# Performance work log

Hardware: AMD Instinct MI355X
Metric: run time of the kernel (lower is better)

## Reference

```python
import jax, jax.numpy as jnp
import numpy as np

N_NODES = 50000
N_EDGES = 600000
D = 128
NUM_GRAPHS = 64


def gcn_conv(x, W, b, edge_index, edge_weight, n):
    """PyG GCNConv: y = D^-1/2 (A+I) D^-1/2 (x W) + b, with self-loop weight 1."""
    h = x @ W  # [n, out]
    src, dst = edge_index[0], edge_index[1]
    if edge_weight is None:
        edge_weight = jnp.ones(src.shape, dtype=x.dtype)
    # append self loops
    loop = jnp.arange(n)
    src_f = jnp.concatenate([src, loop])
    dst_f = jnp.concatenate([dst, loop])
    w_f = jnp.concatenate([edge_weight, jnp.ones((n,), dtype=x.dtype)])
    deg = jax.ops.segment_sum(w_f, dst_f, num_segments=n)
    dis = jnp.where(deg > 0, jax.lax.rsqrt(jnp.maximum(deg, 1e-12)), 0.0)
    norm = dis[src_f] * w_f * dis[dst_f]  # [E+n]
    msg = h[src_f] * norm[:, None]
    out = jax.ops.segment_sum(msg, dst_f, num_segments=n)
    return out + b


def setup_inputs() -> dict:
    key = jax.random.key(0)
    ks = jax.random.split(key, 24)
    def w(k, shape, scale=0.05):
        return jax.random.normal(k, shape, dtype=jnp.float32) * scale
    inp = {
        'x': jax.random.normal(ks[0], (N_NODES, D), dtype=jnp.float32),
        'edge_index': jax.random.randint(ks[1], (2, N_EDGES), 0, N_NODES),
        'edge_attr': jax.random.uniform(ks[2], (N_EDGES, 4), dtype=jnp.float32),
        'batch': jnp.sort(jax.random.randint(ks[3], (N_NODES,), 0, NUM_GRAPHS)),
        'W1A': w(ks[4], (D, D)), 'b1A': jnp.zeros((D,), jnp.float32),
        'W1B': w(ks[5], (D, D)), 'b1B': jnp.zeros((D,), jnp.float32),
        'W1C': w(ks[6], (D, D)), 'b1C': jnp.zeros((D,), jnp.float32),
        'W1D': w(ks[7], (D, D)), 'b1D': jnp.zeros((D,), jnp.float32),
        'W2': w(ks[8], (4 * D, 2 * D)), 'b2': jnp.zeros((2 * D,), jnp.float32),
        'W3': w(ks[9], (2 * D, D)), 'b3': jnp.zeros((D,), jnp.float32),
        'Wm1': w(ks[10], (2 * D, 8)), 'bm1': jnp.zeros((8,), jnp.float32),
        'Wm2': w(ks[11], (8, 2)), 'bm2': jnp.zeros((2,), jnp.float32),
    }
    return inp


def reference(x, edge_index, edge_attr, batch, W1A, b1A, W1B, b1B, W1C, b1C,
              W1D, b1D, W2, b2, W3, b3, Wm1, bm1, Wm2, bm2):
    n = x.shape[0]
    xA = jax.nn.relu(gcn_conv(x, W1A, b1A, edge_index, edge_attr[:, 0], n))
    xB = jax.nn.relu(gcn_conv(x, W1B, b1B, edge_index, edge_attr[:, 1], n))
    xC = jax.nn.relu(gcn_conv(x, W1C, b1C, edge_index, edge_attr[:, 2], n))
    xD = jax.nn.relu(gcn_conv(x, W1D, b1D, edge_index, edge_attr[:, 3], n))
    h = jnp.concatenate([xA, xB, xC, xD], axis=1)  # [n, 4D]
    h = jax.nn.relu(gcn_conv(h, W2, b2, edge_index, None, n))
    h = gcn_conv(h, W3, b3, edge_index, None, n)  # [n, D]
    # global mean / max pool over graphs
    counts = jax.ops.segment_sum(jnp.ones((n,), h.dtype), batch, num_segments=NUM_GRAPHS)
    sums = jax.ops.segment_sum(h, batch, num_segments=NUM_GRAPHS)
    mean = sums / jnp.maximum(counts, 1.0)[:, None]
    mx = jax.ops.segment_max(h, batch, num_segments=NUM_GRAPHS)
    mx = jnp.where(counts[:, None] > 0, mx, 0.0)
    g = jnp.concatenate([mean, mx], axis=1)  # [G, 2D]
    # dropout is identity in eval mode
    logits = jax.nn.relu(g @ Wm1 + bm1) @ Wm2 + bm2
    return logits
```

## Files before the change

### kernel.cpp

```cpp
#include <hip/hip_runtime.h>

#define DEV_INLINE __device__ __forceinline__

typedef __attribute__((ext_vector_type(8))) short bf16x8;
typedef __attribute__((ext_vector_type(4))) float floatx4;

DEV_INLINE unsigned fencode(float f) {
  unsigned u = __float_as_uint(f);
  return (u & 0x80000000u) ? ~u : (u | 0x80000000u);
}
DEV_INLINE float fdecode(unsigned k) {
  return __uint_as_float((k & 0x80000000u) ? (k ^ 0x80000000u) : ~k);
}

DEV_INLINE unsigned short bf16_rne(float x) {
  unsigned u = __float_as_uint(x);
  unsigned r = (u + 0x7FFFu + ((u >> 16) & 1u)) >> 16;
  return (unsigned short)r;
}
DEV_INLINE float bf2f(unsigned short u) {
  return __uint_as_float(((unsigned)u) << 16);
}

#pragma clang diagnostic ignored "-Waddress-space-conversion"
DEV_INLINE void gload_lds16(const void* g, void* l) {
  __builtin_amdgcn_global_load_lds(
      (const __attribute__((address_space(1))) unsigned int*)g,
      (__attribute__((address_space(3))) unsigned int*)l, 16, 0, 0);
}

__global__ __launch_bounds__(256)
void prep_kernel(const float* __restrict__ WA, const float* __restrict__ WB,
                 const float* __restrict__ WC, const float* __restrict__ WD,
                 const float* __restrict__ bA, const float* __restrict__ bB,
                 const float* __restrict__ bC, const float* __restrict__ bD,
                 const float* __restrict__ W2, const float* __restrict__ W3,
                 unsigned short* __restrict__ W1t, unsigned short* __restrict__ W2t,
                 unsigned short* __restrict__ W3t, float* __restrict__ biascat,
                 const float* __restrict__ x, unsigned short* __restrict__ xb,
                 int total4) {
  int i = blockIdx.x * 256 + threadIdx.x;
  if (i < 65536) {
    int z = i >> 14, rem = i & 16383, j = rem >> 7, k = rem & 127;
    const float* W = (z == 0) ? WA : (z == 1) ? WB : (z == 2) ? WC : WD;
    W1t[i] = bf16_rne(W[k * 128 + j]);
  } else if (i < 196608) {
    int i2 = i - 65536, j = i2 >> 9, k = i2 & 511;
    W2t[i2] = bf16_rne(W2[k * 256 + j]);
  } else if (i < 229376) {
    int i3 = i - 196608, j = i3 >> 8, k = i3 & 255;
    W3t[i3] = bf16_rne(W3[k * 128 + j]);
  } else if (i < 229888) {
    int i4 = i - 229376, c = i4 >> 7, j = i4 & 127;
    const float* b = (c == 0) ? bA : (c == 1) ? bB : (c == 2) ? bC : bD;
    biascat[i4] = b[j];
  }
  if (i < total4) {
    float4 v = ((const float4*)x)[i];
    ushort4 o;
    o.x = bf16_rne(v.x); o.y = bf16_rne(v.y); o.z = bf16_rne(v.z); o.w = bf16_rne(v.w);
    ((ushort4*)xb)[i] = o;
  }
}

__global__ __launch_bounds__(256)
void hist_kernel(const int* __restrict__ ei, int* __restrict__ cnt, int E) {
  int e = blockIdx.x * 256 + threadIdx.x;
  if (e < E) atomicAdd(&cnt[ei[E + e]], 1);
}

__global__ __launch_bounds__(256)
void scan1_kernel(const int* __restrict__ cnt, int* __restrict__ local,
                  int* __restrict__ bsum, int n) {
  __shared__ int s[256];
  int tid = threadIdx.x;
  int i = blockIdx.x * 256 + tid;
  int v = (i < n) ? cnt[i] : 0;
  s[tid] = v;
  __syncthreads();
#pragma unroll
  for (int off = 1; off < 256; off <<= 1) {
    int t = (tid >= off) ? s[tid - off] : 0;
    __syncthreads();
    s[tid] += t;
    __syncthreads();
  }
  if (i < n) local[i] = s[tid] - v;
  if (tid == 255) bsum[blockIdx.x] = s[255];
}

__global__ __launch_bounds__(256)
void scan2_kernel(int* __restrict__ bsum, int nb) {
  __shared__ int s[256];
  int tid = threadIdx.x;
  int v = (tid < nb) ? bsum[tid] : 0;
  s[tid] = v;
  __syncthreads();
#pragma unroll
  for (int off = 1; off < 256; off <<= 1) {
    int t = (tid >= off) ? s[tid - off] : 0;
    __syncthreads();
    s[tid] += t;
    __syncthreads();
  }
  if (tid < nb) bsum[tid] = s[tid] - v;
}

__global__ __launch_bounds__(256)
void scan3_kernel(const int* __restrict__ local, const int* __restrict__ bsum,
                  int* __restrict__ rowptr, int* __restrict__ rowwork, int n, int E) {
  int i = blockIdx.x * 256 + threadIdx.x;
  if (i < n) {
    int rp = local[i] + bsum[blockIdx.x];
    rowptr[i] = rp;
    rowwork[i] = rp;
  }
  if (i == 0) rowptr[n] = E;
}

__global__ __launch_bounds__(256)
void fill_kernel(const int* __restrict__ ei, const float* __restrict__ eattr,
                 int* __restrict__ rowwork, int* __restrict__ csr_src,
                 int* __restrict__ csr_dst, float4* __restrict__ csr_w, int E) {
  int e = blockIdx.x * 256 + threadIdx.x;
  if (e >= E) return;
  int d = ei[E + e];
  int pos = atomicAdd(&rowwork[d], 1);
  csr_src[pos] = ei[e];
  csr_dst[pos] = d;
  csr_w[pos] = ((const float4*)eattr)[e];
}

__global__ __launch_bounds__(256)
void degcsr_kernel(const int* __restrict__ rowptr, const float4* __restrict__ csr_w,
                   float* __restrict__ dis, int n) {
  int d = blockIdx.x * 256 + threadIdx.x;
  if (d >= n) return;
  int beg = rowptr[d], end = rowptr[d + 1];
  float s0 = 1.f, s1 = 1.f, s2 = 1.f, s3 = 1.f;
  for (int i = beg; i < end; ++i) {
    float4 w = csr_w[i];
    s0 += w.x; s1 += w.y; s2 += w.z; s3 += w.w;
  }
  dis[d]         = 1.0f / sqrtf(s0);
  dis[n + d]     = 1.0f / sqrtf(s1);
  dis[2 * n + d] = 1.0f / sqrtf(s2);
  dis[3 * n + d] = 1.0f / sqrtf(s3);
  dis[4 * n + d] = 1.0f / sqrtf(1.0f + (float)(end - beg));
}

__global__ __launch_bounds__(256)
void edgeprep_kernel(const int* __restrict__ csr_src, const int* __restrict__ csr_dst,
                     const float4* __restrict__ csr_w, const float* __restrict__ dis,
                     float4* __restrict__ norm4, float* __restrict__ norm1,
                     int n, int E) {
  int i = blockIdx.x * 256 + threadIdx.x;
  if (i >= E) return;
  int s = csr_src[i], d = csr_dst[i];
  float4 w = csr_w[i];
  float4 o;
  o.x = dis[s] * w.x * dis[d];
  o.y = dis[n + s] * w.y * dis[n + d];
  o.z = dis[2 * n + s] * w.z * dis[2 * n + d];
  o.w = dis[3 * n + s] * w.w * dis[3 * n + d];
  norm4[i] = o;
  norm1[i] = dis[4 * n + s] * dis[4 * n + d];
}

__global__ __launch_bounds__(256)
void agg4x_kernel(const unsigned short* __restrict__ xb,
                  unsigned short* __restrict__ xa,
                  const int* __restrict__ rowptr, const int* __restrict__ csr_src,
                  const float4* __restrict__ norm4, const float* __restrict__ dis,
                  int n, int npad) {
  int d = blockIdx.x * 4 + (threadIdx.x >> 6);
  if (d >= n) return;
  int t = threadIdx.x & 63;
  float dc0 = dis[d], dc1 = dis[n + d], dc2 = dis[2 * n + d], dc3 = dis[3 * n + d];
  const ushort2* x2 = (const ushort2*)xb;
  ushort2 xu = x2[(size_t)d * 64 + t];
  float xvx = bf2f(xu.x), xvy = bf2f(xu.y);
  float a0x = xvx * dc0 * dc0, a0y = xvy * dc0 * dc0;
  float a1x = xvx * dc1 * dc1, a1y = xvy * dc1 * dc1;
  float a2x = xvx * dc2 * dc2, a2y = xvy * dc2 * dc2;
  float a3x = xvx * dc3 * dc3, a3y = xvy * dc3 * dc3;
  int beg = rowptr[d], end = rowptr[d + 1];
  int i = beg;
  for (; i + 4 <= end; i += 4) {
    int s0 = csr_src[i], s1 = csr_src[i + 1], s2 = csr_src[i + 2], s3 = csr_src[i + 3];
    float4 m0 = norm4[i], m1 = norm4[i + 1], m2 = norm4[i + 2], m3 = norm4[i + 3];
    ushort2 u0 = x2[(size_t)s0 * 64 + t];
    ushort2 u1 = x2[(size_t)s1 * 64 + t];
    ushort2 u2 = x2[(size_t)s2 * 64 + t];
    ushort2 u3 = x2[(size_t)s3 * 64 + t];
    float h0x = bf2f(u0.x), h0y = bf2f(u0.y);
    float h1x = bf2f(u1.x), h1y = bf2f(u1.y);
    float h2x = bf2f(u2.x), h2y = bf2f(u2.y);
    float h3x = bf2f(u3.x), h3y = bf2f(u3.y);
    a0x += h0x * m0.x; a0y += h0y * m0.x;
    a1x += h0x * m0.y; a1y += h0y * m0.y;
    a2x += h0x * m0.z; a2y += h0y * m0.z;
    a3x += h0x * m0.w; a3y += h0y * m0.w;
    a0x += h1x * m1.x; a0y += h1y * m1.x;
    a1x += h1x * m1.y; a1y += h1y * m1.y;
    a2x += h1x * m1.z; a2y += h1y * m1.z;
    a3x += h1x * m1.w; a3y += h1y * m1.w;
    a0x += h2x * m2.x; a0y += h2y * m2.x;
    a1x += h2x * m2.y; a1y += h2y * m2.y;
    a2x += h2x * m2.z; a2y += h2y * m2.z;
    a3x += h2x * m2.w; a3y += h2y * m2.w;
    a0x += h3x * m3.x; a0y += h3y * m3.x;
    a1x += h3x * m3.y; a1y += h3y * m3.y;
    a2x += h3x * m3.z; a2y += h3y * m3.z;
    a3x += h3x * m3.w; a3y += h3y * m3.w;
  }
  for (; i < end; ++i) {
    int s = csr_src[i];
    float4 m = norm4[i];
    ushort2 u = x2[(size_t)s * 64 + t];
    float hx = bf2f(u.x), hy = bf2f(u.y);
    a0x += hx * m.x; a0y += hy * m.x;
    a1x += hx * m.y; a1y += hy * m.y;
    a2x += hx * m.z; a2y += hy * m.z;
    a3x += hx * m.w; a3y += hy * m.w;
  }
  size_t plane = (size_t)npad * 128;
  size_t base = (size_t)d * 128 + 2 * t;
  float vx[4] = {a0x, a1x, a2x, a3x};
  float vy[4] = {a0y, a1y, a2y, a3y};
#pragma unroll
  for (int z = 0; z < 4; ++z) {
    ushort2 ov; ov.x = bf16_rne(vx[z]); ov.y = bf16_rne(vy[z]);
    *(ushort2*)&xa[plane * z + base] = ov;
  }
}

template <int MODE>
DEV_INLINE void gemm_mfma_body(const unsigned short* __restrict__ A, int K,
                               const unsigned short* __restrict__ B,
                               int ldc, int col0, unsigned short* __restrict__ Cb,
                               const float* __restrict__ bias, int M, int row0) {
  __shared__ __align__(16) unsigned short As[2][128 * 32];
  __shared__ __align__(16) unsigned short Bs[2][128 * 32];
  int tid = threadIdx.x;
  int w = tid >> 6, lane = tid & 63;
  int quad = lane >> 4, lrow = lane & 15;
  int wm = (w >> 1) * 64, wn = (w & 1) * 64;

  floatx4 acc[4][4];
#pragma unroll
  for (int i = 0; i < 4; ++i)
#pragma unroll
    for (int j = 0; j < 4; ++j) acc[i][j] = {0.f, 0.f, 0.f, 0.f};

  auto stage = [&](int b, int k0) {
#pragma unroll
    for (int half = 0; half < 2; ++half) {
      int row = half * 64 + lane;
      int lb = (w * 128 + half * 64) * 8;
      gload_lds16(A + (size_t)(row0 + row) * K + k0 + w * 8, &As[b][lb]);
      gload_lds16(B + (size_t)row * K + k0 + w * 8, &Bs[b][lb]);
    }
  };

  int nk = K >> 5;
  stage(0, 0);
  int buf = 0;
  for (int kt = 0; kt < nk; ++kt) {
    __syncthreads();
    if (kt + 1 < nk) stage(buf ^ 1, (kt + 1) * 32);
    bf16x8 a_[4], b_[4];
#pragma unroll
    for (int i = 0; i < 4; ++i)
      a_[i] = *(const bf16x8*)&As[buf][(quad * 128 + wm + i * 16 + lrow) * 8];
#pragma unroll
    for (int j = 0; j < 4; ++j)
      b_[j] = *(const bf16x8*)&Bs[buf][(quad * 128 + wn + j * 16 + lrow) * 8];
#pragma unroll
    for (int j = 0; j < 4; ++j)
#pragma unroll
      for (int i = 0; i < 4; ++i)
        acc[i][j] = __builtin_amdgcn_mfma_f32_16x16x32_bf16(a_[i], b_[j], acc[i][j], 0, 0, 0);
    buf ^= 1;
  }
#pragma unroll
  for (int i = 0; i < 4; ++i) {
#pragma unroll
    for (int j = 0; j < 4; ++j) {
      int colL = wn + j * 16 + lrow;
#pragma unroll
      for (int r = 0; r < 4; ++r) {
        int row = row0 + wm + i * 16 + quad * 4 + r;
        if (row < M) {
          float v = acc[i][j][r];
          if (MODE == 1) v = fmaxf(v + bias[colL], 0.0f);
          Cb[(size_t)row * ldc + col0 + colL] = bf16_rne(v);
        }
      }
    }
  }
}

__global__ __launch_bounds__(256)
void gemm_l1_mfma(const unsigned short* __restrict__ xa,
                  const unsigned short* __restrict__ W1t,
                  const float* __restrict__ biascat,
                  unsigned short* __restrict__ h1, int M, int npad) {
  int z = blockIdx.z;
  gemm_mfma_body<1>(xa + (size_t)z * npad * 128, 128, W1t + z * 16384,
                    512, z * 128, h1, biascat + z * 128, M, blockIdx.x * 128);
}

__global__ __launch_bounds__(256)
void gemm_bf16out(const unsigned short* __restrict__ A, int K,
                  const unsigned short* __restrict__ B,
                  unsigned short* __restrict__ Cb, int ldc, int M) {
  gemm_mfma_body<2>(A, K, B + (size_t)blockIdx.y * 128 * K, ldc,
                    blockIdx.y * 128, Cb, nullptr, M, blockIdx.x * 128);
}

__global__ __launch_bounds__(512)
void gemm_l2_wide(const unsigned short* __restrict__ A,
                  const unsigned short* __restrict__ B,
                  unsigned short* __restrict__ Cb, int M) {
  constexpr int K = 512;
  __shared__ __align__(16) unsigned short As[2][128 * 32];
  __shared__ __align__(16) unsigned short Bs[2][256 * 32];
  int tid = threadIdx.x;
  int w = tid >> 6, lane = tid & 63;
  int quad = lane >> 4, lrow = lane & 15;
  int wm = (w >> 2) * 64, wn = (w & 3) * 64;
  int row0 = blockIdx.x * 128;
  int u0 = w * 64;

  floatx4 acc[4][4];
#pragma unroll
  for (int i = 0; i < 4; ++i)
#pragma unroll
    for (int j = 0; j < 4; ++j) acc[i][j] = {0.f, 0.f, 0.f, 0.f};

  auto stage = [&](int b, int k0) {
    gload_lds16(A + (size_t)(row0 + (tid & 127)) * K + k0 + (tid >> 7) * 8,
                &As[b][u0 * 8]);
#pragma unroll
    for (int inst = 0; inst < 2; ++inst) {
      int u = inst * 512 + tid;
      gload_lds16(B + (size_t)(u & 255) * K + k0 + (u >> 8) * 8,
                  &Bs[b][(inst * 512 + u0) * 8]);
    }
  };

  stage(0, 0);
  int buf = 0;
#pragma unroll 1
  for (int kt = 0; kt < 16; ++kt) {
    __syncthreads();
    if (kt + 1 < 16) stage(buf ^ 1, (kt + 1) * 32);
    bf16x8 a_[4], b_[4];
#pragma unroll
    for (int i = 0; i < 4; ++i)
      a_[i] = *(const bf16x8*)&As[buf][(quad * 128 + wm + i * 16 + lrow) * 8];
#pragma unroll
    for (int j = 0; j < 4; ++j)
      b_[j] = *(const bf16x8*)&Bs[buf][(quad * 256 + wn + j * 16 + lrow) * 8];
#pragma unroll
    for (int j = 0; j < 4; ++j)
#pragma unroll
      for (int i = 0; i < 4; ++i)
        acc[i][j] = __builtin_amdgcn_mfma_f32_16x16x32_bf16(a_[i], b_[j], acc[i][j], 0, 0, 0);
    buf ^= 1;
  }
#pragma unroll
  for (int i = 0; i < 4; ++i) {
#pragma unroll
    for (int j = 0; j < 4; ++j) {
      int colL = wn + j * 16 + lrow;
#pragma unroll
      for (int r = 0; r < 4; ++r) {
        int row = row0 + wm + i * 16 + quad * 4 + r;
        if (row < M) Cb[(size_t)row * 256 + colL] = bf16_rne(acc[i][j][r]);
      }
    }
  }
}

template <int VEC, bool RELU, int OMODE>
__global__ __launch_bounds__(256)
void agg1_kernel(const unsigned short* __restrict__ hb, float* __restrict__ out,
                 unsigned short* __restrict__ ob,
                 const int* __restrict__ rowptr, const int* __restrict__ csr_src,
                 const float* __restrict__ norm1, const float* __restrict__ dis1,
                 const float* __restrict__ bias, int n) {
  constexpr int DOUT = VEC * 64;
  int d = blockIdx.x * 4 + (threadIdx.x >> 6);
  if (d >= n) return;
  int t = threadIdx.x & 63;
  float dd = dis1[d];
  float acc[VEC];
  {
    float sw = dd * dd;
#pragma unroll
    for (int k = 0; k < VEC; ++k) acc[k] = bf2f(hb[(size_t)d * DOUT + t * VEC + k]) * sw;
  }
  int beg = rowptr[d], end = rowptr[d + 1];
  int i = beg;
  for (; i + 4 <= end; i += 4) {
    int s0 = csr_src[i], s1 = csr_src[i + 1], s2 = csr_src[i + 2], s3 = csr_src[i + 3];
    float m0 = norm1[i], m1 = norm1[i + 1], m2 = norm1[i + 2], m3 = norm1[i + 3];
    if (VEC == 4) {
      ushort4 u0 = *(const ushort4*)&hb[(size_t)s0 * DOUT + t * 4];
      ushort4 u1 = *(const ushort4*)&hb[(size_t)s1 * DOUT + t * 4];
      ushort4 u2 = *(const ushort4*)&hb[(size_t)s2 * DOUT + t * 4];
      ushort4 u3 = *(const ushort4*)&hb[(size_t)s3 * DOUT + t * 4];
      acc[0] += bf2f(u0.x) * m0; acc[1] += bf2f(u0.y) * m0;
      acc[2 % VEC] += bf2f(u0.z) * m0; acc[3 % VEC] += bf2f(u0.w) * m0;
      acc[0] += bf2f(u1.x) * m1; acc[1] += bf2f(u1.y) * m1;
      acc[2 % VEC] += bf2f(u1.z) * m1; acc[3 % VEC] += bf2f(u1.w) * m1;
      acc[0] += bf2f(u2.x) * m2; acc[1] += bf2f(u2.y) * m2;
      acc[2 % VEC] += bf2f(u2.z) * m2; acc[3 % VEC] += bf2f(u2.w) * m2;
      acc[0] += bf2f(u3.x) * m3; acc[1] += bf2f(u3.y) * m3;
      acc[2 % VEC] += bf2f(u3.z) * m3; acc[3 % VEC] += bf2f(u3.w) * m3;
    } else {
      ushort2 u0 = *(const ushort2*)&hb[(size_t)s0 * DOUT + t * 2];
      ushort2 u1 = *(const ushort2*)&hb[(size_t)s1 * DOUT + t * 2];
      ushort2 u2 = *(const ushort2*)&hb[(size_t)s2 * DOUT + t * 2];
      ushort2 u3 = *(const ushort2*)&hb[(size_t)s3 * DOUT + t * 2];
      acc[0] += bf2f(u0.x) * m0; acc[1 % VEC] += bf2f(u0.y) * m0;
      acc[0] += bf2f(u1.x) * m1; acc[1 % VEC] += bf2f(u1.y) * m1;
      acc[0] += bf2f(u2.x) * m2; acc[1 % VEC] += bf2f(u2.y) * m2;
      acc[0] += bf2f(u3.x) * m3; acc[1 % VEC] += bf2f(u3.y) * m3;
    }
  }
  for (; i < end; ++i) {
    int s = csr_src[i];
    float nrm = norm1[i];
    if (VEC == 4) {
      ushort4 u = *(const ushort4*)&hb[(size_t)s * DOUT + t * 4];
      acc[0] += bf2f(u.x) * nrm; acc[1] += bf2f(u.y) * nrm;
      acc[2 % VEC] += bf2f(u.z) * nrm; acc[3 % VEC] += bf2f(u.w) * nrm;
    } else {
      ushort2 u = *(const ushort2*)&hb[(size_t)s * DOUT + t * 2];
      acc[0] += bf2f(u.x) * nrm; acc[1 % VEC] += bf2f(u.y) * nrm;
    }
  }
#pragma unroll
  for (int k = 0; k < VEC; ++k) {
    float r = acc[k] + bias[t * VEC + k];
    if (RELU) r = fmaxf(r, 0.0f);
    if (OMODE == 1) {
      ob[(size_t)d * DOUT + t * VEC + k] = bf16_rne(r);
    } else {
      out[(size_t)d * DOUT + t * VEC + k] = r;
    }
  }
}

__global__ __launch_bounds__(128)
void pool_kernel(const float* __restrict__ h3, const int* __restrict__ batch,
                 float* __restrict__ gsum, unsigned* __restrict__ gmax, int n) {
  int c = threadIdx.x;
  int start = blockIdx.x * 32;
  int end = min(start + 32, n);
  int curg = -1;
  float s = 0.0f, m = -3.402823466e38f;
  for (int i = start; i < end; ++i) {
    int g = batch[i];
    if (g != curg) {
      if (curg >= 0) {
        atomicAdd(&gsum[curg * 128 + c], s);
        atomicMax(&gmax[curg * 128 + c], fencode(m));
      }
      curg = g; s = 0.0f; m = -3.402823466e38f;
    }
    float v = h3[(size_t)i * 128 + c];
    s += v;
    m = fmaxf(m, v);
  }
  if (curg >= 0) {
    atomicAdd(&gsum[curg * 128 + c], s);
    atomicMax(&gmax[curg * 128 + c], fencode(m));
  }
}

__global__ __launch_bounds__(512)
void mlp_kernel(const float* __restrict__ gsum, const unsigned* __restrict__ gmax,
                const int* __restrict__ batch, int n, const float* __restrict__ Wm1,
                const float* __restrict__ bm1, const float* __restrict__ Wm2,
                const float* __restrict__ bm2, float* __restrict__ out) {
  __shared__ float hid[64][8];
  int t = threadIdx.x;
  int gi = t >> 3, u = t & 7;
  auto lb = [&](int key) {
    int lo = 0, hi = n;
    while (lo < hi) {
      int mid = (lo + hi) >> 1;
      if (batch[mid] < key) lo = mid + 1; else hi = mid;
    }
    return lo;
  };
  int cnt = lb(gi + 1) - lb(gi);
  float inv = 1.0f / fmaxf((float)cnt, 1.0f);
  float s = bm1[u];
  for (int k = 0; k < 128; ++k) {
    float mean = gsum[gi * 128 + k] * inv;
    s += mean * Wm1[k * 8 + u];
  }
  for (int k = 0; k < 128; ++k) {
    float mx = (cnt > 0) ? fdecode(gmax[gi * 128 + k]) : 0.0f;
    s += mx * Wm1[(128 + k) * 8 + u];
  }
  hid[gi][u] = fmaxf(s, 0.0f);
  __syncthreads();
  if (t < 128) {
    int g2 = t >> 1, o = t & 1;
    float s2 = bm2[o];
#pragma unroll
    for (int uu = 0; uu < 8; ++uu) s2 += hid[g2][uu] * Wm2[uu * 2 + o];
    out[g2 * 2 + o] = s2;
  }
}

extern "C" void kernel_launch(void* const* d_in, const int* in_sizes, int n_in,
                              void* d_out, int out_size, void* d_ws, size_t ws_size,
                              hipStream_t stream) {
  const float* x     = (const float*)d_in[0];
  const int*   ei    = (const int*)d_in[1];
  const float* eattr = (const float*)d_in[2];
  const int*   batch = (const int*)d_in[3];
  const float* W1A = (const float*)d_in[4],  *b1A = (const float*)d_in[5];
  const float* W1B = (const float*)d_in[6],  *b1B = (const float*)d_in[7];
  const float* W1C = (const float*)d_in[8],  *b1C = (const float*)d_in[9];
  const float* W1D = (const float*)d_in[10], *b1D = (const float*)d_in[11];
  const float* W2  = (const float*)d_in[12], *b2  = (const float*)d_in[13];
  const float* W3  = (const float*)d_in[14], *b3  = (const float*)d_in[15];
  const float* Wm1 = (const float*)d_in[16], *bm1 = (const float*)d_in[17];
  const float* Wm2 = (const float*)d_in[18], *bm2 = (const float*)d_in[19];
  float* out = (float*)d_out;

  const int n = in_sizes[0] / 128;
  const int E = in_sizes[1] / 2;
  const int npad = (n + 127) & ~127;
  const int nmb = npad / 128;

  char* ws = (char*)d_ws;
  size_t off = 0;
  auto alloc = [&](size_t bytes) -> void* {
    void* p = ws + off;
    off += (bytes + 255) & ~(size_t)255;
    return p;
  };

  float*    dis     = (float*)alloc((size_t)5 * n * 4);
  int*      rowptr  = (int*)alloc(((size_t)n + 1) * 4);
  int*      rowwork = (int*)alloc((size_t)n * 4);
  int*      local   = (int*)alloc((size_t)n * 4);
  int*      bsum    = (int*)alloc(256 * 4);
  size_t zoff = off;
  int*      cnt     = (int*)alloc((size_t)n * 4);
  float*    gsum    = (float*)alloc(64 * 128 * 4);
  unsigned* gmax    = (unsigned*)alloc(64 * 128 * 4);
  size_t zbytes = off - zoff;
  int*      csr_src = (int*)alloc((size_t)E * 4);
  int*      csr_dst = (int*)alloc((size_t)E * 4);
  float4*   csr_w   = (float4*)alloc((size_t)E * 16);
  float4*   norm4   = (float4*)alloc((size_t)E * 16);
  float*    norm1   = (float*)alloc((size_t)E * 4);
  unsigned short* W1t = (unsigned short*)alloc(65536 * 2);
  unsigned short* W2t = (unsigned short*)alloc(131072 * 2);
  unsigned short* W3t = (unsigned short*)alloc(32768 * 2);
  float*    biascat = (float*)alloc(512 * 4);
  unsigned short* xb   = (unsigned short*)alloc((size_t)npad * 128 * 2);
  unsigned short* bufA = (unsigned short*)alloc((size_t)npad * 512 * 2);
  unsigned short* bufB = (unsigned short*)alloc((size_t)npad * 512 * 2);
  alloc(4096);

  unsigned short* xa      = bufA;
  unsigned short* h1      = bufB;
  unsigned short* h2pre_b = bufA;
  unsigned short* h2      = bufB;
  unsigned short* h3pre_b = bufA;
  float*          h3      = (float*)(bufB + (size_t)npad * 256);

  hipMemsetAsync(ws + zoff, 0, zbytes, stream);

  int total4 = n * 32;
  prep_kernel<<<(total4 + 255) / 256, 256, 0, stream>>>(
      W1A, W1B, W1C, W1D, b1A, b1B, b1C, b1D, W2, W3,
      W1t, W2t, W3t, biascat, x, xb, total4);

  int nb = (n + 255) / 256;
  hist_kernel<<<(E + 255) / 256, 256, 0, stream>>>(ei, cnt, E);
  scan1_kernel<<<nb, 256, 0, stream>>>(cnt, local, bsum, n);
  scan2_kernel<<<1, 256, 0, stream>>>(bsum, nb);
  scan3_kernel<<<nb, 256, 0, stream>>>(local, bsum, rowptr, rowwork, n, E);
  fill_kernel<<<(E + 255) / 256, 256, 0, stream>>>(ei, eattr, rowwork, csr_src, csr_dst, csr_w, E);
  degcsr_kernel<<<(n + 255) / 256, 256, 0, stream>>>(rowptr, csr_w, dis, n);
  edgeprep_kernel<<<(E + 255) / 256, 256, 0, stream>>>(csr_src, csr_dst, csr_w,
                                                       dis, norm4, norm1, n, E);

  int nodeblk = (n + 3) / 4;
  agg4x_kernel<<<nodeblk, 256, 0, stream>>>(xb, xa, rowptr, csr_src, norm4, dis, n, npad);
  gemm_l1_mfma<<<dim3(nmb, 1, 4), 256, 0, stream>>>(xa, W1t, biascat, h1, n, npad);
  gemm_l2_wide<<<nmb, 512, 0, stream>>>(h1, W2t, h2pre_b, n);
  agg1_kernel<4, true, 1><<<nodeblk, 256, 0, stream>>>(h2pre_b, nullptr, h2,
                                                       rowptr, csr_src, norm1,
                                                       dis + (size_t)4 * n, b2, n);
  gemm_bf16out<<<dim3(nmb, 1), 256, 0, stream>>>(h2, 256, W3t, h3pre_b, 128, n);
  agg1_kernel<2, false, 0><<<nodeblk, 256, 0, stream>>>(h3pre_b, h3, nullptr,
                                                        rowptr, csr_src, norm1,
                                                        dis + (size_t)4 * n, b3, n);

  pool_kernel<<<(n + 31) / 32, 128, 0, stream>>>(h3, batch, gsum, gmax, n);
  mlp_kernel<<<1, 512, 0, stream>>>(gsum, gmax, batch, n, Wm1, bm1, Wm2, bm2, out);
}
```

Before: 477.3 us.

## Specialize layer-1 GEMM with full-K LDS load and split layer-2 aggregation

Layer-1 GEMM gets its own kernel that loads the whole K=128 A and B tiles into LDS at once, with no double-buffered k-loop, and applies bias+ReLU inline. The layer-2 aggregation over 256 columns is split into two 128-column passes with a stride parameter, which shrinks the per-row gather footprint and may improve cache locality. The final aggregation now writes bf16 instead of fp32, and pooling reads bf16, which halves that traffic at some cost in precision. The bigger LDS footprint (64KB per block) can lower occupancy for the GEMM, and the second pass re-reads the CSR arrays.

```diff
diff --git a/kernel.cpp b/kernel.cpp
--- a/kernel.cpp
+++ b/kernel.cpp
@@ -235,11 +235,79 @@
   }
 }
 
-template <int MODE>
-DEV_INLINE void gemm_mfma_body(const unsigned short* __restrict__ A, int K,
-                               const unsigned short* __restrict__ B,
-                               int ldc, int col0, unsigned short* __restrict__ Cb,
-                               const float* __restrict__ bias, int M, int row0) {
+__global__ __launch_bounds__(256)
+void gemm_l1_mfma(const unsigned short* __restrict__ xa,
+                  const unsigned short* __restrict__ W1t,
+                  const float* __restrict__ biascat,
+                  unsigned short* __restrict__ h1, int M, int npad) {
+  int z = blockIdx.z;
+  const unsigned short* A = xa + (size_t)z * npad * 128;
+  const unsigned short* B = W1t + z * 16384;
+  __shared__ __align__(16) unsigned short As[128 * 128];
+  __shared__ __align__(16) unsigned short Bs[128 * 128];
+  int tid = threadIdx.x;
+  int w = tid >> 6, lane = tid & 63;
+  int quad = lane >> 4, lrow = lane & 15;
+  int wm = (w >> 1) * 64, wn = (w & 1) * 64;
+  int row0 = blockIdx.x * 128;
+
+#pragma unroll
+  for (int u4q = 0; u4q < 4; ++u4q) {
+    int u4 = w * 4 + u4q;
+#pragma unroll
+    for (int half = 0; half < 2; ++half) {
+      int row = half * 64 + lane;
+      int lb = (u4 * 128 + half * 64) * 8;
+      gload_lds16(A + (size_t)(row0 + row) * 128 + u4 * 8, &As[lb]);
+      gload_lds16(B + (size_t)row * 128 + u4 * 8, &Bs[lb]);
+    }
+  }
+  __syncthreads();
+
+  floatx4 acc[4][4];
+#pragma unroll
+  for (int i = 0; i < 4; ++i)
+#pragma unroll
+    for (int j = 0; j < 4; ++j) acc[i][j] = {0.f, 0.f, 0.f, 0.f};
+
+#pragma unroll
+  for (int kc = 0; kc < 4; ++kc) {
+    bf16x8 a_[4], b_[4];
+#pragma unroll
+    for (int i = 0; i < 4; ++i)
+      a_[i] = *(const bf16x8*)&As[((kc * 4 + quad) * 128 + wm + i * 16 + lrow) * 8];
+#pragma unroll
+    for (int j = 0; j < 4; ++j)
+      b_[j] = *(const bf16x8*)&Bs[((kc * 4 + quad) * 128 + wn + j * 16 + lrow) * 8];
+#pragma unroll
+    for (int j = 0; j < 4; ++j)
+#pragma unroll
+      for (int i = 0; i < 4; ++i)
+        acc[i][j] = __builtin_amdgcn_mfma_f32_16x16x32_bf16(a_[i], b_[j], acc[i][j], 0, 0, 0);
+  }
+#pragma unroll
+  for (int i = 0; i < 4; ++i) {
+#pragma unroll
+    for (int j = 0; j < 4; ++j) {
+      int colL = wn + j * 16 + lrow;
+#pragma unroll
+      for (int r = 0; r < 4; ++r) {
+        int row = row0 + wm + i * 16 + quad * 4 + r;
+        if (row < M) {
+          float v = fmaxf(acc[i][j][r] + biascat[z * 128 + colL], 0.0f);
+          h1[(size_t)row * 512 + z * 128 + colL] = bf16_rne(v);
+        }
+      }
+    }
+  }
+}
+
+__global__ __launch_bounds__(256)
+void gemm_bf16out(const unsigned short* __restrict__ A, int K,
+                  const unsigned short* __restrict__ Bfull,
+                  unsigned short* __restrict__ Cb, int ldc, int M) {
+  const unsigned short* B = Bfull + (size_t)blockIdx.y * 128 * K;
+  int col0 = blockIdx.y * 128, row0 = blockIdx.x * 128;
   __shared__ __align__(16) unsigned short As[2][128 * 32];
   __shared__ __align__(16) unsigned short Bs[2][128 * 32];
   int tid = threadIdx.x;
@@ -291,32 +359,10 @@
 #pragma unroll
       for (int r = 0; r < 4; ++r) {
         int row = row0 + wm + i * 16 + quad * 4 + r;
-        if (row < M) {
-          float v = acc[i][j][r];
-          if (MODE == 1) v = fmaxf(v + bias[colL], 0.0f);
-          Cb[(size_t)row * ldc + col0 + colL] = bf16_rne(v);
-        }
+        if (row < M) Cb[(size_t)row * ldc + col0 + colL] = bf16_rne(acc[i][j][r]);
       }
     }
   }
-}
-
-__global__ __launch_bounds__(256)
-void gemm_l1_mfma(const unsigned short* __restrict__ xa,
-                  const unsigned short* __restrict__ W1t,
-                  const float* __restrict__ biascat,
-                  unsigned short* __restrict__ h1, int M, int npad) {
-  int z = blockIdx.z;
-  gemm_mfma_body<1>(xa + (size_t)z * npad * 128, 128, W1t + z * 16384,
-                    512, z * 128, h1, biascat + z * 128, M, blockIdx.x * 128);
-}
-
-__global__ __launch_bounds__(256)
-void gemm_bf16out(const unsigned short* __restrict__ A, int K,
-                  const unsigned short* __restrict__ B,
-                  unsigned short* __restrict__ Cb, int ldc, int M) {
-  gemm_mfma_body<2>(A, K, B + (size_t)blockIdx.y * 128 * K, ldc,
-                    blockIdx.y * 128, Cb, nullptr, M, blockIdx.x * 128);
 }
 
 __global__ __launch_bounds__(512)
@@ -384,79 +430,52 @@
   }
 }
 
-template <int VEC, bool RELU, int OMODE>
-__global__ __launch_bounds__(256)
-void agg1_kernel(const unsigned short* __restrict__ hb, float* __restrict__ out,
+template <bool RELU>
+__global__ __launch_bounds__(256)
+void agg1_kernel(const unsigned short* __restrict__ hb, int ldh,
                  unsigned short* __restrict__ ob,
                  const int* __restrict__ rowptr, const int* __restrict__ csr_src,
                  const float* __restrict__ norm1, const float* __restrict__ dis1,
                  const float* __restrict__ bias, int n) {
-  constexpr int DOUT = VEC * 64;
   int d = blockIdx.x * 4 + (threadIdx.x >> 6);
   if (d >= n) return;
   int t = threadIdx.x & 63;
   float dd = dis1[d];
-  float acc[VEC];
+  float a0, a1;
   {
     float sw = dd * dd;
-#pragma unroll
-    for (int k = 0; k < VEC; ++k) acc[k] = bf2f(hb[(size_t)d * DOUT + t * VEC + k]) * sw;
+    ushort2 u = *(const ushort2*)&hb[(size_t)d * ldh + 2 * t];
+    a0 = bf2f(u.x) * sw; a1 = bf2f(u.y) * sw;
   }
   int beg = rowptr[d], end = rowptr[d + 1];
   int i = beg;
   for (; i + 4 <= end; i += 4) {
     int s0 = csr_src[i], s1 = csr_src[i + 1], s2 = csr_src[i + 2], s3 = csr_src[i + 3];
     float m0 = norm1[i], m1 = norm1[i + 1], m2 = norm1[i + 2], m3 = norm1[i + 3];
-    if (VEC == 4) {
-      ushort4 u0 = *(const ushort4*)&hb[(size_t)s0 * DOUT + t * 4];
-      ushort4 u1 = *(const ushort4*)&hb[(size_t)s1 * DOUT + t * 4];
-      ushort4 u2 = *(const ushort4*)&hb[(size_t)s2 * DOUT + t * 4];
-      ushort4 u3 = *(const ushort4*)&hb[(size_t)s3 * DOUT + t * 4];
-      acc[0] += bf2f(u0.x) * m0; acc[1] += bf2f(u0.y) * m0;
-      acc[2 % VEC] += bf2f(u0.z) * m0; acc[3 % VEC] += bf2f(u0.w) * m0;
-      acc[0] += bf2f(u1.x) * m1; acc[1] += bf2f(u1.y) * m1;
-      acc[2 % VEC] += bf2f(u1.z) * m1; acc[3 % VEC] += bf2f(u1.w) * m1;
-      acc[0] += bf2f(u2.x) * m2; acc[1] += bf2f(u2.y) * m2;
-      acc[2 % VEC] += bf2f(u2.z) * m2; acc[3 % VEC] += bf2f(u2.w) * m2;
-      acc[0] += bf2f(u3.x) * m3; acc[1] += bf2f(u3.y) * m3;
-      acc[2 % VEC] += bf2f(u3.z) * m3; acc[3 % VEC] += bf2f(u3.w) * m3;
-    } else {
-      ushort2 u0 = *(const ushort2*)&hb[(size_t)s0 * DOUT + t * 2];
-      ushort2 u1 = *(const ushort2*)&hb[(size_t)s1 * DOUT + t * 2];
-      ushort2 u2 = *(const ushort2*)&hb[(size_t)s2 * DOUT + t * 2];
-      ushort2 u3 = *(const ushort2*)&hb[(size_t)s3 * DOUT + t * 2];
-      acc[0] += bf2f(u0.x) * m0; acc[1 % VEC] += bf2f(u0.y) * m0;
-      acc[0] += bf2f(u1.x) * m1; acc[1 % VEC] += bf2f(u1.y) * m1;
-      acc[0] += bf2f(u2.x) * m2; acc[1 % VEC] += bf2f(u2.y) * m2;
-      acc[0] += bf2f(u3.x) * m3; acc[1 % VEC] += bf2f(u3.y) * m3;
-    }
+    ushort2 u0 = *(const ushort2*)&hb[(size_t)s0 * ldh + 2 * t];
+    ushort2 u1 = *(const ushort2*)&hb[(size_t)s1 * ldh + 2 * t];
+    ushort2 u2 = *(const ushort2*)&hb[(size_t)s2 * ldh + 2 * t];
+    ushort2 u3 = *(const ushort2*)&hb[(size_t)s3 * ldh + 2 * t];
+    a0 += bf2f(u0.x) * m0; a1 += bf2f(u0.y) * m0;
+    a0 += bf2f(u1.x) * m1; a1 += bf2f(u1.y) * m1;
+    a0 += bf2f(u2.x) * m2; a1 += bf2f(u2.y) * m2;
+    a0 += bf2f(u3.x) * m3; a1 += bf2f(u3.y) * m3;
   }
   for (; i < end; ++i) {
     int s = csr_src[i];
     float nrm = norm1[i];
-    if (VEC == 4) {
-      ushort4 u = *(const ushort4*)&hb[(size_t)s * DOUT + t * 4];
-      acc[0] += bf2f(u.x) * nrm; acc[1] += bf2f(u.y) * nrm;
-      acc[2 % VEC] += bf2f(u.z) * nrm; acc[3 % VEC] += bf2f(u.w) * nrm;
-    } else {
-      ushort2 u = *(const ushort2*)&hb[(size_t)s * DOUT + t * 2];
-      acc[0] += bf2f(u.x) * nrm; acc[1 % VEC] += bf2f(u.y) * nrm;
-    }
-  }
-#pragma unroll
-  for (int k = 0; k < VEC; ++k) {
-    float r = acc[k] + bias[t * VEC + k];
-    if (RELU) r = fmaxf(r, 0.0f);
-    if (OMODE == 1) {
-      ob[(size_t)d * DOUT + t * VEC + k] = bf16_rne(r);
-    } else {
-      out[(size_t)d * DOUT + t * VEC + k] = r;
-    }
-  }
+    ushort2 u = *(const ushort2*)&hb[(size_t)s * ldh + 2 * t];
+    a0 += bf2f(u.x) * nrm; a1 += bf2f(u.y) * nrm;
+  }
+  float r0 = a0 + bias[2 * t];
+  float r1 = a1 + bias[2 * t + 1];
+  if (RELU) { r0 = fmaxf(r0, 0.0f); r1 = fmaxf(r1, 0.0f); }
+  ushort2 ov; ov.x = bf16_rne(r0); ov.y = bf16_rne(r1);
+  *(ushort2*)&ob[(size_t)d * ldh + 2 * t] = ov;
 }
 
 __global__ __launch_bounds__(128)
-void pool_kernel(const float* __restrict__ h3, const int* __restrict__ batch,
+void pool_kernel(const unsigned short* __restrict__ h3b, const int* __restrict__ batch,
                  float* __restrict__ gsum, unsigned* __restrict__ gmax, int n) {
   int c = threadIdx.x;
   int start = blockIdx.x * 32;
@@ -472,7 +491,7 @@
       }
       curg = g; s = 0.0f; m = -3.402823466e38f;
     }
-    float v = h3[(size_t)i * 128 + c];
+    float v = bf2f(h3b[(size_t)i * 128 + c]);
     s += v;
     m = fmaxf(m, v);
   }
@@ -579,7 +598,7 @@
   unsigned short* h2pre_b = bufA;
   unsigned short* h2      = bufB;
   unsigned short* h3pre_b = bufA;
-  float*          h3      = (float*)(bufB + (size_t)npad * 256);
+  unsigned short* h3b     = bufB + (size_t)npad * 256;
 
   hipMemsetAsync(ws + zoff, 0, zbytes, stream);
 
@@ -599,17 +618,18 @@
                                                        dis, norm4, norm1, n, E);
 
   int nodeblk = (n + 3) / 4;
+  const float* dis5 = dis + (size_t)4 * n;
   agg4x_kernel<<<nodeblk, 256, 0, stream>>>(xb, xa, rowptr, csr_src, norm4, dis, n, npad);
   gemm_l1_mfma<<<dim3(nmb, 1, 4), 256, 0, stream>>>(xa, W1t, biascat, h1, n, npad);
   gemm_l2_wide<<<nmb, 512, 0, stream>>>(h1, W2t, h2pre_b, n);
-  agg1_kernel<4, true, 1><<<nodeblk, 256, 0, stream>>>(h2pre_b, nullptr, h2,
-                                                       rowptr, csr_src, norm1,
-                                                       dis + (size_t)4 * n, b2, n);
+  agg1_kernel<true><<<nodeblk, 256, 0, stream>>>(h2pre_b, 256, h2,
+                                                 rowptr, csr_src, norm1, dis5, b2, n);
+  agg1_kernel<true><<<nodeblk, 256, 0, stream>>>(h2pre_b + 128, 256, h2 + 128,
+                                                 rowptr, csr_src, norm1, dis5, b2 + 128, n);
   gemm_bf16out<<<dim3(nmb, 1), 256, 0, stream>>>(h2, 256, W3t, h3pre_b, 128, n);
-  agg1_kernel<2, false, 0><<<nodeblk, 256, 0, stream>>>(h3pre_b, h3, nullptr,
-                                                        rowptr, csr_src, norm1,
-                                                        dis + (size_t)4 * n, b3, n);
-
-  pool_kernel<<<(n + 31) / 32, 128, 0, stream>>>(h3, batch, gsum, gmax, n);
+  agg1_kernel<false><<<nodeblk, 256, 0, stream>>>(h3pre_b, 128, h3b,
+                                                  rowptr, csr_src, norm1, dis5, b3, n);
+
+  pool_kernel<<<(n + 31) / 32, 128, 0, stream>>>(h3b, batch, gsum, gmax, n);
   mlp_kernel<<<1, 512, 0, stream>>>(gsum, gmax, batch, n, Wm1, bm1, Wm2, bm2, out);
 }
```

New measurement: 500.4 us. +4.8%, slower.

## Fuse degree computation into histogram and edge norms into CSR fill

Applied to the files above, without the earlier changes.

Per-destination weighted degrees are now accumulated with float atomics in the histogram pass, and the inverse square roots are computed in the final scan pass. Each edge's normalisation is then computed directly in the CSR fill kernel. This drops the degcsr and edgeprep kernels along with the csr_dst and csr_w arrays, saving two launches and the extra edge-array traffic. As a separate change, the last aggregation output is stored as bf16 instead of fp32 before pooling. The costs are four extra float atomics per edge, nondeterministic summation order, and some precision loss in h3.

```diff
diff --git a/kernel.cpp b/kernel.cpp
--- a/kernel.cpp
+++ b/kernel.cpp
@@ -64,9 +64,17 @@
 }
 
 __global__ __launch_bounds__(256)
-void hist_kernel(const int* __restrict__ ei, int* __restrict__ cnt, int E) {
+void hist_kernel(const int* __restrict__ ei, const float* __restrict__ eattr,
+                 int* __restrict__ cnt, float* __restrict__ dis, int n, int E) {
   int e = blockIdx.x * 256 + threadIdx.x;
-  if (e < E) atomicAdd(&cnt[ei[E + e]], 1);
+  if (e >= E) return;
+  int d = ei[E + e];
+  atomicAdd(&cnt[d], 1);
+  float4 w = ((const float4*)eattr)[e];
+  atomicAdd(&dis[d], w.x);
+  atomicAdd(&dis[n + d], w.y);
+  atomicAdd(&dis[2 * n + d], w.z);
+  atomicAdd(&dis[3 * n + d], w.w);
 }
 
 __global__ __launch_bounds__(256)
@@ -108,12 +116,18 @@
 
 __global__ __launch_bounds__(256)
 void scan3_kernel(const int* __restrict__ local, const int* __restrict__ bsum,
-                  int* __restrict__ rowptr, int* __restrict__ rowwork, int n, int E) {
+                  const int* __restrict__ cnt, int* __restrict__ rowptr,
+                  int* __restrict__ rowwork, float* __restrict__ dis, int n, int E) {
   int i = blockIdx.x * 256 + threadIdx.x;
   if (i < n) {
     int rp = local[i] + bsum[blockIdx.x];
     rowptr[i] = rp;
     rowwork[i] = rp;
+    dis[i]         = 1.0f / sqrtf(1.0f + dis[i]);
+    dis[n + i]     = 1.0f / sqrtf(1.0f + dis[n + i]);
+    dis[2 * n + i] = 1.0f / sqrtf(1.0f + dis[2 * n + i]);
+    dis[3 * n + i] = 1.0f / sqrtf(1.0f + dis[3 * n + i]);
+    dis[4 * n + i] = 1.0f / sqrtf(1.0f + (float)cnt[i]);
   }
   if (i == 0) rowptr[n] = E;
 }
@@ -121,50 +135,21 @@
 __global__ __launch_bounds__(256)
 void fill_kernel(const int* __restrict__ ei, const float* __restrict__ eattr,
                  int* __restrict__ rowwork, int* __restrict__ csr_src,
-                 int* __restrict__ csr_dst, float4* __restrict__ csr_w, int E) {
+                 float4* __restrict__ norm4, float* __restrict__ norm1,
+                 const float* __restrict__ dis, int n, int E) {
   int e = blockIdx.x * 256 + threadIdx.x;
   if (e >= E) return;
-  int d = ei[E + e];
+  int s = ei[e], d = ei[E + e];
   int pos = atomicAdd(&rowwork[d], 1);
-  csr_src[pos] = ei[e];
-  csr_dst[pos] = d;
-  csr_w[pos] = ((const float4*)eattr)[e];
-}
-
-__global__ __launch_bounds__(256)
-void degcsr_kernel(const int* __restrict__ rowptr, const float4* __restrict__ csr_w,
-                   float* __restrict__ dis, int n) {
-  int d = blockIdx.x * 256 + threadIdx.x;
-  if (d >= n) return;
-  int beg = rowptr[d], end = rowptr[d + 1];
-  float s0 = 1.f, s1 = 1.f, s2 = 1.f, s3 = 1.f;
-  for (int i = beg; i < end; ++i) {
-    float4 w = csr_w[i];
-    s0 += w.x; s1 += w.y; s2 += w.z; s3 += w.w;
-  }
-  dis[d]         = 1.0f / sqrtf(s0);
-  dis[n + d]     = 1.0f / sqrtf(s1);
-  dis[2 * n + d] = 1.0f / sqrtf(s2);
-  dis[3 * n + d] = 1.0f / sqrtf(s3);
-  dis[4 * n + d] = 1.0f / sqrtf(1.0f + (float)(end - beg));
-}
-
-__global__ __launch_bounds__(256)
-void edgeprep_kernel(const int* __restrict__ csr_src, const int* __restrict__ csr_dst,
-                     const float4* __restrict__ csr_w, const float* __restrict__ dis,
-                     float4* __restrict__ norm4, float* __restrict__ norm1,
-                     int n, int E) {
-  int i = blockIdx.x * 256 + threadIdx.x;
-  if (i >= E) return;
-  int s = csr_src[i], d = csr_dst[i];
-  float4 w = csr_w[i];
+  csr_src[pos] = s;
+  float4 w = ((const float4*)eattr)[e];
   float4 o;
   o.x = dis[s] * w.x * dis[d];
   o.y = dis[n + s] * w.y * dis[n + d];
   o.z = dis[2 * n + s] * w.z * dis[2 * n + d];
   o.w = dis[3 * n + s] * w.w * dis[3 * n + d];
-  norm4[i] = o;
-  norm1[i] = dis[4 * n + s] * dis[4 * n + d];
+  norm4[pos] = o;
+  norm1[pos] = dis[4 * n + s] * dis[4 * n + d];
 }
 
 __global__ __launch_bounds__(256)
@@ -384,9 +369,9 @@
   }
 }
 
-template <int VEC, bool RELU, int OMODE>
-__global__ __launch_bounds__(256)
-void agg1_kernel(const unsigned short* __restrict__ hb, float* __restrict__ out,
+template <int VEC, bool RELU>
+__global__ __launch_bounds__(256)
+void agg1_kernel(const unsigned short* __restrict__ hb,
                  unsigned short* __restrict__ ob,
                  const int* __restrict__ rowptr, const int* __restrict__ csr_src,
                  const float* __restrict__ norm1, const float* __restrict__ dis1,
@@ -447,16 +432,12 @@
   for (int k = 0; k < VEC; ++k) {
     float r = acc[k] + bias[t * VEC + k];
     if (RELU) r = fmaxf(r, 0.0f);
-    if (OMODE == 1) {
-      ob[(size_t)d * DOUT + t * VEC + k] = bf16_rne(r);
-    } else {
-      out[(size_t)d * DOUT + t * VEC + k] = r;
-    }
+    ob[(size_t)d * DOUT + t * VEC + k] = bf16_rne(r);
   }
 }
 
 __global__ __launch_bounds__(128)
-void pool_kernel(const float* __restrict__ h3, const int* __restrict__ batch,
+void pool_kernel(const unsigned short* __restrict__ h3b, const int* __restrict__ batch,
                  float* __restrict__ gsum, unsigned* __restrict__ gmax, int n) {
   int c = threadIdx.x;
   int start = blockIdx.x * 32;
@@ -472,7 +453,7 @@
       }
       curg = g; s = 0.0f; m = -3.402823466e38f;
     }
-    float v = h3[(size_t)i * 128 + c];
+    float v = bf2f(h3b[(size_t)i * 128 + c]);
     s += v;
     m = fmaxf(m, v);
   }
@@ -550,19 +531,17 @@
     return p;
   };
 
-  float*    dis     = (float*)alloc((size_t)5 * n * 4);
   int*      rowptr  = (int*)alloc(((size_t)n + 1) * 4);
   int*      rowwork = (int*)alloc((size_t)n * 4);
   int*      local   = (int*)alloc((size_t)n * 4);
   int*      bsum    = (int*)alloc(256 * 4);
   size_t zoff = off;
+  float*    dis     = (float*)alloc((size_t)5 * n * 4);
   int*      cnt     = (int*)alloc((size_t)n * 4);
   float*    gsum    = (float*)alloc(64 * 128 * 4);
   unsigned* gmax    = (unsigned*)alloc(64 * 128 * 4);
   size_t zbytes = off - zoff;
   int*      csr_src = (int*)alloc((size_t)E * 4);
-  int*      csr_dst = (int*)alloc((size_t)E * 4);
-  float4*   csr_w   = (float4*)alloc((size_t)E * 16);
   float4*   norm4   = (float4*)alloc((size_t)E * 16);
   float*    norm1   = (float*)alloc((size_t)E * 4);
   unsigned short* W1t = (unsigned short*)alloc(65536 * 2);
@@ -579,7 +558,7 @@
   unsigned short* h2pre_b = bufA;
   unsigned short* h2      = bufB;
   unsigned short* h3pre_b = bufA;
-  float*          h3      = (float*)(bufB + (size_t)npad * 256);
+  unsigned short* h3b     = bufB + (size_t)npad * 256;
 
   hipMemsetAsync(ws + zoff, 0, zbytes, stream);
 
@@ -589,27 +568,24 @@
       W1t, W2t, W3t, biascat, x, xb, total4);
 
   int nb = (n + 255) / 256;
-  hist_kernel<<<(E + 255) / 256, 256, 0, stream>>>(ei, cnt, E);
+  hist_kernel<<<(E + 255) / 256, 256, 0, stream>>>(ei, eattr, cnt, dis, n, E);
   scan1_kernel<<<nb, 256, 0, stream>>>(cnt, local, bsum, n);
   scan2_kernel<<<1, 256, 0, stream>>>(bsum, nb);
-  scan3_kernel<<<nb, 256, 0, stream>>>(local, bsum, rowptr, rowwork, n, E);
-  fill_kernel<<<(E + 255) / 256, 256, 0, stream>>>(ei, eattr, rowwork, csr_src, csr_dst, csr_w, E);
-  degcsr_kernel<<<(n + 255) / 256, 256, 0, stream>>>(rowptr, csr_w, dis, n);
-  edgeprep_kernel<<<(E + 255) / 256, 256, 0, stream>>>(csr_src, csr_dst, csr_w,
-                                                       dis, norm4, norm1, n, E);
+  scan3_kernel<<<nb, 256, 0, stream>>>(local, bsum, cnt, rowptr, rowwork, dis, n, E);
+  fill_kernel<<<(E + 255) / 256, 256, 0, stream>>>(ei, eattr, rowwork, csr_src,
+                                                   norm4, norm1, dis, n, E);
 
   int nodeblk = (n + 3) / 4;
+  const float* dis5 = dis + (size_t)4 * n;
   agg4x_kernel<<<nodeblk, 256, 0, stream>>>(xb, xa, rowptr, csr_src, norm4, dis, n, npad);
   gemm_l1_mfma<<<dim3(nmb, 1, 4), 256, 0, stream>>>(xa, W1t, biascat, h1, n, npad);
   gemm_l2_wide<<<nmb, 512, 0, stream>>>(h1, W2t, h2pre_b, n);
-  agg1_kernel<4, true, 1><<<nodeblk, 256, 0, stream>>>(h2pre_b, nullptr, h2,
-                                                       rowptr, csr_src, norm1,
-                                                       dis + (size_t)4 * n, b2, n);
+  agg1_kernel<4, true><<<nodeblk, 256, 0, stream>>>(h2pre_b, h2, rowptr, csr_src,
+                                                    norm1, dis5, b2, n);
   gemm_bf16out<<<dim3(nmb, 1), 256, 0, stream>>>(h2, 256, W3t, h3pre_b, 128, n);
-  agg1_kernel<2, false, 0><<<nodeblk, 256, 0, stream>>>(h3pre_b, h3, nullptr,
-                                                        rowptr, csr_src, norm1,
-                                                        dis + (size_t)4 * n, b3, n);
-
-  pool_kernel<<<(n + 31) / 32, 128, 0, stream>>>(h3, batch, gsum, gmax, n);
+  agg1_kernel<2, false><<<nodeblk, 256, 0, stream>>>(h3pre_b, h3b, rowptr, csr_src,
+                                                     norm1, dis5, b3, n);
+
+  pool_kernel<<<(n + 31) / 32, 128, 0, stream>>>(h3b, batch, gsum, gmax, n);
   mlp_kernel<<<1, 512, 0, stream>>>(gsum, gmax, batch, n, Wm1, bm1, Wm2, bm2, out);
 }
```

Measured after the change: 567.0 us. 1.19x slower.
